# Kernel optimization log

Measured on AMD Instinct MI355X. Metric: run time of the kernel, lower is better.

Reference implementation:

```python
import jax, jax.numpy as jnp
import numpy as np

N = 100000   # nodes
E = 625000   # edges
D = 128      # feature dim (layers = [128,128,128])
H = 8        # attention heads
HD = 16      # head dim (H*HD == D)


def setup_inputs() -> dict:
    key = jax.random.key(0)
    ks = jax.random.split(key, 16)
    s = 1.0 / np.sqrt(D).astype(np.float32)
    inp = {
        'x': jax.random.normal(ks[0], (N, D), dtype=jnp.float32),
        'edge_index': jax.random.randint(ks[1], (2, E), 0, N, dtype=jnp.int64),
        'W1': jax.random.normal(ks[2], (D, D), dtype=jnp.float32) * s,
        'b1': jnp.zeros((D,), jnp.float32),
        'W2': jax.random.normal(ks[3], (D, D), dtype=jnp.float32) * s,
        'b2': jnp.zeros((D,), jnp.float32),
        'Wq': jax.random.normal(ks[4], (D, H * HD), dtype=jnp.float32) * s,
        'bq': jnp.zeros((H * HD,), jnp.float32),
        'Wk': jax.random.normal(ks[5], (D, H * HD), dtype=jnp.float32) * s,
        'bk': jnp.zeros((H * HD,), jnp.float32),
        'Wv': jax.random.normal(ks[6], (D, H * HD), dtype=jnp.float32) * s,
        'bv': jnp.zeros((H * HD,), jnp.float32),
        'Wo': jax.random.normal(ks[7], (H * HD, D), dtype=jnp.float32) * s,
        'bo': jnp.zeros((D,), jnp.float32),
    }
    return inp


def _gcn_conv(x, W, b, src, dst):
    """PyG GCNConv: x' = D^-1/2 (A+I) D^-1/2 (x W) + b, symmetric norm with self-loops."""
    h = x @ W                                   # [N, Dout]
    # degree at targets, +1 for self-loop
    deg = jnp.ones((N,), h.dtype).at[dst].add(jnp.ones((E,), h.dtype))
    dinv = jax.lax.rsqrt(deg)                   # [N]
    norm = dinv[src] * dinv[dst]                # [E]
    agg = jnp.zeros_like(h).at[dst].add(h[src] * norm[:, None])
    agg = agg + h * (dinv * dinv)[:, None]      # self-loop term
    return agg + b


def _mha_seq1(x, Wq, bq, Wk, bk, Wv, bv, Wo, bo):
    """Faithful to the hand-rolled MHA: batch=N, implied seq_len=1."""
    n = x.shape[0]
    q = (x @ Wq + bq).reshape(n, 1, H, HD).transpose(0, 2, 1, 3)  # [N,H,1,HD]
    k = (x @ Wk + bk).reshape(n, 1, H, HD).transpose(0, 2, 1, 3)
    v = (x @ Wv + bv).reshape(n, 1, H, HD).transpose(0, 2, 1, 3)
    scores = jnp.einsum('nhqd,nhkd->nhqk', q, k) / np.float32(np.sqrt(HD))
    attn = jax.nn.softmax(scores, axis=-1)                        # [N,H,1,1]
    out = jnp.einsum('nhqk,nhkd->nhqd', attn, v)                  # [N,H,1,HD]
    out = out.transpose(0, 2, 1, 3).reshape(n, 1, H * HD)
    return out @ Wo + bo                                          # [N,1,D]


def reference(x, edge_index, W1, b1, W2, b2, Wq, bq, Wk, bk, Wv, bv, Wo, bo):
    src, dst = edge_index[0], edge_index[1]
    h = _gcn_conv(x, W1, b1, src, dst)
    h = jax.nn.relu(h)                 # dropout is identity in eval
    h = _gcn_conv(h, W2, b2, src, dst) # last conv: no relu
    return _mha_seq1(h, Wq, bq, Wk, bk, Wv, bv, Wo, bo)
```

## Files before the change

### kernel.cpp

```cpp
#include <hip/hip_runtime.h>
#include <hip/hip_bf16.h>

#define DD 128
#define CAP 16
#define OVF_MAX 8192
#define ECHUNK 2048

typedef __bf16 bf16x8v __attribute__((ext_vector_type(8)));
typedef float  f32x4   __attribute__((ext_vector_type(4)));

__device__ inline unsigned short f2bf(float f) {
    unsigned u = __builtin_bit_cast(unsigned, f);
    unsigned r = (u + 0x7fffu + ((u >> 16) & 1u)) >> 16;
    return (unsigned short)r;
}
__device__ inline float bflo2f(unsigned p) { return __builtin_bit_cast(float, p << 16); }
__device__ inline float bfhi2f(unsigned p) { return __builtin_bit_cast(float, p & 0xffff0000u); }
__device__ inline float rl_f(int v, int i) {
    return __builtin_bit_cast(float, __builtin_amdgcn_readlane(v, i));
}

__global__ __launch_bounds__(256) void k_zero(int* __restrict__ a, int N) {
    int i = blockIdx.x * 256 + threadIdx.x;
    int stride = gridDim.x * 256;
    for (; i <= N; i += stride) a[i] = 0;
}

__global__ __launch_bounds__(256) void k_fill_fuse1(const int* __restrict__ src, const int* __restrict__ dst,
                                                    int* __restrict__ fillc, int* __restrict__ srcp,
                                                    int* __restrict__ ovfcnt, int2* __restrict__ ovf,
                                                    int E, int N, int FB,
                                                    const float* __restrict__ Wv, const float* __restrict__ Wo,
                                                    const float* __restrict__ bv, const float* __restrict__ bo,
                                                    float* __restrict__ Wf, float* __restrict__ bfo) {
    if ((int)blockIdx.x < FB) {
        int bin   = blockIdx.x & 7;
        int chunk = blockIdx.x >> 3;
        int binsz = (N + 7) / 8;
        int lo = bin * binsz;
        int hi = lo + binsz; if (hi > N) hi = N;
        int base = chunk * ECHUNK + threadIdx.x;
        #pragma unroll
        for (int i = 0; i < ECHUNK / 256; ++i) {
            int e = base + i * 256;
            if (e < E) {
                int d = dst[e];
                if (d >= lo && d < hi) {
                    int s = src[e];
                    if ((unsigned)s < (unsigned)N) {
                        int pos = atomicAdd(&fillc[d], 1);
                        if (pos < CAP) srcp[(size_t)d * CAP + pos] = s;
                        else {
                            int op = atomicAdd(ovfcnt, 1);
                            if (op < OVF_MAX) ovf[op] = make_int2(s, d);
                        }
                    }
                }
            }
        }
    } else {
        int gid = (blockIdx.x - FB) * 256 + threadIdx.x;
        if (gid >= (DD + 1) * DD) return;
        int i = gid >> 7, j = gid & (DD - 1);
        if (i < DD) {
            float acc = 0.f;
            for (int k = 0; k < DD; ++k) acc = fmaf(Wv[i * DD + k], Wo[k * DD + j], acc);
            Wf[i * DD + j] = acc;
        } else {
            float acc = bo[j];
            for (int k = 0; k < DD; ++k) acc = fmaf(bv[k], Wo[k * DD + j], acc);
            bfo[j] = acc;
        }
    }
}

__global__ __launch_bounds__(256) void k_dinv_wprep(const int* __restrict__ fillc, float* __restrict__ dinv,
                                                    int N, int nb,
                                                    const float* __restrict__ W2, const float* __restrict__ Wf,
                                                    const float* __restrict__ b2, const float* __restrict__ bfo,
                                                    unsigned short* __restrict__ W2ft, float* __restrict__ bf2,
                                                    const float* __restrict__ W1, unsigned short* __restrict__ Wt1) {
    if ((int)blockIdx.x < nb) {
        int n = blockIdx.x * 256 + threadIdx.x;
        if (n < N) dinv[n] = rsqrtf(1.0f + (float)fillc[n]);
    } else {
        int blk = blockIdx.x - nb;
        if (blk < 65) {
            int gid = blk * 256 + threadIdx.x;
            if (gid >= (DD + 1) * DD) return;
            int i = gid >> 7, j = gid & (DD - 1);
            if (i < DD) {
                float acc = 0.f;
                for (int k = 0; k < DD; ++k) acc = fmaf(W2[i * DD + k], Wf[k * DD + j], acc);
                W2ft[j * DD + i] = f2bf(acc);
            } else {
                float acc = bfo[j];
                for (int k = 0; k < DD; ++k) acc = fmaf(b2[k], Wf[k * DD + j], acc);
                bf2[j] = acc;
            }
        } else {
            int gid = (blk - 65) * 256 + threadIdx.x;
            int k = gid >> 7, n = gid & 127;
            Wt1[n * DD + k] = f2bf(W1[k * DD + n]);
        }
    }
}

template<int AF32>
__global__ __launch_bounds__(256, 2) void k_gemm_mfma(const void* __restrict__ Av,
                                                      const unsigned short* __restrict__ Wt,
                                                      unsigned short* __restrict__ Cb, int M) {
    int w  = threadIdx.x >> 6;
    int l  = threadIdx.x & 63;
    int lr = l & 15, lg = l >> 4;

    bf16x8v bfr[8][4];
    #pragma unroll
    for (int nt = 0; nt < 8; ++nt)
        #pragma unroll
        for (int kk = 0; kk < 4; ++kk)
            bfr[nt][kk] = *reinterpret_cast<const bf16x8v*>(Wt + (nt * 16 + lr) * DD + kk * 32 + lg * 8);

    int tiles = (M + 63) >> 6;
    for (int t = blockIdx.x; t < tiles; t += gridDim.x) {
        int m0 = t * 64 + w * 16;
        int row = m0 + lr;
        int rowc = row < M ? row : (M - 1);

        bf16x8v af[4];
        if (AF32) {
            const float* Af = (const float*)Av;
            #pragma unroll
            for (int kk = 0; kk < 4; ++kk) {
                const float* p = Af + (size_t)rowc * DD + kk * 32 + lg * 8;
                float4 u0 = *reinterpret_cast<const float4*>(p);
                float4 u1 = *reinterpret_cast<const float4*>(p + 4);
                af[kk][0] = (__bf16)u0.x; af[kk][1] = (__bf16)u0.y;
                af[kk][2] = (__bf16)u0.z; af[kk][3] = (__bf16)u0.w;
                af[kk][4] = (__bf16)u1.x; af[kk][5] = (__bf16)u1.y;
                af[kk][6] = (__bf16)u1.z; af[kk][7] = (__bf16)u1.w;
            }
        } else {
            const unsigned short* Ab = (const unsigned short*)Av;
            #pragma unroll
            for (int kk = 0; kk < 4; ++kk)
                af[kk] = *reinterpret_cast<const bf16x8v*>(Ab + (size_t)rowc * DD + kk * 32 + lg * 8);
        }

        f32x4 acc[8] = {};
        #pragma unroll
        for (int kk = 0; kk < 4; ++kk)
            #pragma unroll
            for (int nt = 0; nt < 8; ++nt)
                acc[nt] = __builtin_amdgcn_mfma_f32_16x16x32_bf16(af[kk], bfr[nt][kk], acc[nt], 0, 0, 0);

        #pragma unroll
        for (int nt = 0; nt < 8; ++nt)
            #pragma unroll
            for (int r = 0; r < 4; ++r) {
                int rr = m0 + lg * 4 + r;
                if (rr < M) Cb[(size_t)rr * DD + nt * 16 + lr] = f2bf(acc[nt][r]);
            }
    }
}

template<int OUTF32, int RELU>
__global__ __launch_bounds__(256) void k_gather_pad(const int* __restrict__ fillc, const int* __restrict__ srcp,
                                                    const float* __restrict__ dinv, const unsigned* __restrict__ h32,
                                                    const float* __restrict__ bias, void* __restrict__ outp,
                                                    int N, const int* __restrict__ ovfcnt, const int2* __restrict__ ovf) {
    int l = threadIdx.x & 63;
    int g = blockIdx.x * 4 + (threadIdx.x >> 6);
    int m0 = g * 4;
    if (m0 >= N) return;
    float2 bb = reinterpret_cast<const float2*>(bias)[l];

    int fcidx = m0 + l; if (fcidx >= N) fcidx = N - 1;
    int fc = (l < 4) ? fillc[fcidx] : 0;

    int deg[4], c[4], sv[4], wvb[4];
    #pragma unroll
    for (int r = 0; r < 4; ++r) {
        deg[r] = __builtin_amdgcn_readlane(fc, r);
        int cc = deg[r] > CAP ? CAP : deg[r];
        c[r] = cc;
        int row = (m0 + r < N) ? (m0 + r) : (N - 1);
        sv[r] = (cc > 0) ? srcp[(size_t)row * CAP + (l < cc ? l : cc - 1)] : 0;
    }
    #pragma unroll
    for (int r = 0; r < 4; ++r)
        wvb[r] = __builtin_bit_cast(int, dinv[sv[r]]);

    unsigned p[4][8]; float w[4][8];
    #pragma unroll
    for (int r = 0; r < 4; ++r) {
        int f = c[r] < 8 ? c[r] : 8;
        #pragma unroll
        for (int q = 0; q < 8; ++q) {
            int i = (q < f) ? q : (f > 0 ? f - 1 : 0);
            int s = __builtin_amdgcn_readlane(sv[r], i);
            p[r][q] = h32[(size_t)s * 64 + l];
            w[r][q] = (q < f) ? rl_f(wvb[r], i) : 0.f;
        }
    }
    unsigned ps[4];
    #pragma unroll
    for (int r = 0; r < 4; ++r) {
        int n = m0 + r; int nc = n < N ? n : N - 1;
        ps[r] = h32[(size_t)nc * 64 + l];
    }

    float ax[4] = {0.f, 0.f, 0.f, 0.f}, ay[4] = {0.f, 0.f, 0.f, 0.f};
    #pragma unroll
    for (int r = 0; r < 4; ++r)
        #pragma unroll
        for (int q = 0; q < 8; ++q) {
            ax[r] = fmaf(w[r][q], bflo2f(p[r][q]), ax[r]);
            ay[r] = fmaf(w[r][q], bfhi2f(p[r][q]), ay[r]);
        }

    #pragma unroll
    for (int r = 0; r < 4; ++r) {
        for (int i = 8; i < c[r]; i += 8) {
            #pragma unroll
            for (int q = 0; q < 8; ++q) {
                int ii = (i + q < c[r]) ? i + q : c[r] - 1;
                int s = __builtin_amdgcn_readlane(sv[r], ii);
                unsigned pp = h32[(size_t)s * 64 + l];
                float wq = (i + q < c[r]) ? rl_f(wvb[r], ii) : 0.f;
                ax[r] = fmaf(wq, bflo2f(pp), ax[r]);
                ay[r] = fmaf(wq, bfhi2f(pp), ay[r]);
            }
        }
    }

    int anyovf = 0;
    #pragma unroll
    for (int r = 0; r < 4; ++r) anyovf |= (deg[r] > CAP) ? 1 : 0;
    if (anyovf) {
        int oc = *ovfcnt; if (oc > OVF_MAX) oc = OVF_MAX;
        for (int i = 0; i < oc; ++i) {
            int2 e = ovf[i];
            #pragma unroll
            for (int r = 0; r < 4; ++r) {
                if (deg[r] > CAP && e.y == m0 + r) {
                    float wq = dinv[e.x];
                    unsigned pp = h32[(size_t)e.x * 64 + l];
                    ax[r] = fmaf(wq, bflo2f(pp), ax[r]);
                    ay[r] = fmaf(wq, bfhi2f(pp), ay[r]);
                }
            }
        }
    }

    #pragma unroll
    for (int r = 0; r < 4; ++r) {
        int n = m0 + r;
        if (n < N) {
            float di = rsqrtf(1.0f + (float)deg[r]);
            float di2 = di * di;
            float ox = fmaf(di2, bflo2f(ps[r]), di * ax[r]) + bb.x;
            float oy = fmaf(di2, bfhi2f(ps[r]), di * ay[r]) + bb.y;
            if (RELU) { ox = fmaxf(ox, 0.f); oy = fmaxf(oy, 0.f); }
            if (OUTF32) {
                reinterpret_cast<float2*>(outp)[(size_t)n * 64 + l] = make_float2(ox, oy);
            } else {
                unsigned po = (unsigned)f2bf(ox) | ((unsigned)f2bf(oy) << 16);
                reinterpret_cast<unsigned*>(outp)[(size_t)n * 64 + l] = po;
            }
        }
    }
}

extern "C" void kernel_launch(void* const* d_in, const int* in_sizes, int n_in,
                              void* d_out, int out_size, void* d_ws, size_t ws_size,
                              hipStream_t stream) {
    const float* x  = (const float*)d_in[0];
    const int*   ei = (const int*)d_in[1];
    const float* W1 = (const float*)d_in[2];
    const float* b1 = (const float*)d_in[3];
    const float* W2 = (const float*)d_in[4];
    const float* b2 = (const float*)d_in[5];
    const float* Wv = (const float*)d_in[10];
    const float* bv = (const float*)d_in[11];
    const float* Wo = (const float*)d_in[12];
    const float* bo = (const float*)d_in[13];
    int N = in_sizes[0] / DD;
    int E = in_sizes[1] / 2;
    const int* src = ei;
    const int* dst = ei + E;
    float* out = (float*)d_out;

    unsigned* hA  = (unsigned*)d_ws;
    unsigned* h1  = hA + (size_t)N * 64;
    float* dinv   = (float*)(h1 + (size_t)N * 64);
    float* Wf     = dinv + N;
    float* bfo    = Wf + DD * DD;
    float* bf2    = bfo + DD;
    unsigned short* Wt1  = (unsigned short*)(bf2 + DD);
    unsigned short* W2ft = Wt1 + DD * DD;
    int* fillc  = (int*)(W2ft + DD * DD);
    int* ovfcnt = fillc + N;
    int2* ovf   = (int2*)(((uintptr_t)(ovfcnt + 1) + 63) & ~(uintptr_t)63);
    int* srcp   = (int*)(((uintptr_t)(ovf + OVF_MAX) + 63) & ~(uintptr_t)63);

    int nb = (N + 255) / 256;
    int nchunks = (E + ECHUNK - 1) / ECHUNK;
    int FB = nchunks * 8;

    k_zero<<<512, 256, 0, stream>>>(fillc, N);
    k_fill_fuse1<<<FB + 129, 256, 0, stream>>>(src, dst, fillc, srcp, ovfcnt, ovf, E, N, FB,
                                               Wv, Wo, bv, bo, Wf, bfo);
    k_dinv_wprep<<<nb + 129, 256, 0, stream>>>(fillc, dinv, N, nb,
                                               W2, Wf, b2, bfo, W2ft, bf2, W1, Wt1);
    k_gemm_mfma<1><<<512, 256, 0, stream>>>(x, Wt1, (unsigned short*)hA, N);
    int nwaves = (N + 3) / 4;
    int gb = (nwaves + 3) / 4;
    k_gather_pad<0, 1><<<gb, 256, 0, stream>>>(fillc, srcp, dinv, hA, b1, h1, N, ovfcnt, ovf);
    k_gemm_mfma<0><<<512, 256, 0, stream>>>(h1, W2ft, (unsigned short*)hA, N);
    k_gather_pad<1, 0><<<gb, 256, 0, stream>>>(fillc, srcp, dinv, hA, bf2, out, N, ovfcnt, ovf);
}
```

Before: 165.8 us.

## Fuse first GCN gather with second-layer GEMM via LDS-staged MFMA

Merges the layer-1 aggregation kernel with the following W2 GEMM. Each 256-thread block aggregates 16 rows into shared memory as bf16, then runs MFMA against the full 128x128 weight matrix staged in LDS. This removes the h1 global round trip and one kernel launch. In exchange, every block reloads the 32KB weight tile from global/L2, and the larger LDS footprint (about 39KB per block) may lower occupancy for a latency-bound gather.

```diff
diff --git a/kernel.cpp b/kernel.cpp
--- a/kernel.cpp
+++ b/kernel.cpp
@@ -106,8 +106,7 @@
     }
 }
 
-template<int AF32>
-__global__ __launch_bounds__(256, 2) void k_gemm_mfma(const void* __restrict__ Av,
+__global__ __launch_bounds__(256, 2) void k_gemm_mfma(const float* __restrict__ Af,
                                                       const unsigned short* __restrict__ Wt,
                                                       unsigned short* __restrict__ Cb, int M) {
     int w  = threadIdx.x >> 6;
@@ -128,23 +127,15 @@
         int rowc = row < M ? row : (M - 1);
 
         bf16x8v af[4];
-        if (AF32) {
-            const float* Af = (const float*)Av;
-            #pragma unroll
-            for (int kk = 0; kk < 4; ++kk) {
-                const float* p = Af + (size_t)rowc * DD + kk * 32 + lg * 8;
-                float4 u0 = *reinterpret_cast<const float4*>(p);
-                float4 u1 = *reinterpret_cast<const float4*>(p + 4);
-                af[kk][0] = (__bf16)u0.x; af[kk][1] = (__bf16)u0.y;
-                af[kk][2] = (__bf16)u0.z; af[kk][3] = (__bf16)u0.w;
-                af[kk][4] = (__bf16)u1.x; af[kk][5] = (__bf16)u1.y;
-                af[kk][6] = (__bf16)u1.z; af[kk][7] = (__bf16)u1.w;
-            }
-        } else {
-            const unsigned short* Ab = (const unsigned short*)Av;
-            #pragma unroll
-            for (int kk = 0; kk < 4; ++kk)
-                af[kk] = *reinterpret_cast<const bf16x8v*>(Ab + (size_t)rowc * DD + kk * 32 + lg * 8);
+        #pragma unroll
+        for (int kk = 0; kk < 4; ++kk) {
+            const float* p = Af + (size_t)rowc * DD + kk * 32 + lg * 8;
+            float4 u0 = *reinterpret_cast<const float4*>(p);
+            float4 u1 = *reinterpret_cast<const float4*>(p + 4);
+            af[kk][0] = (__bf16)u0.x; af[kk][1] = (__bf16)u0.y;
+            af[kk][2] = (__bf16)u0.z; af[kk][3] = (__bf16)u0.w;
+            af[kk][4] = (__bf16)u1.x; af[kk][5] = (__bf16)u1.y;
+            af[kk][6] = (__bf16)u1.z; af[kk][7] = (__bf16)u1.w;
         }
 
         f32x4 acc[8] = {};
@@ -164,17 +155,28 @@
     }
 }
 
-template<int OUTF32, int RELU>
-__global__ __launch_bounds__(256) void k_gather_pad(const int* __restrict__ fillc, const int* __restrict__ srcp,
-                                                    const float* __restrict__ dinv, const unsigned* __restrict__ h32,
-                                                    const float* __restrict__ bias, void* __restrict__ outp,
-                                                    int N, const int* __restrict__ ovfcnt, const int2* __restrict__ ovf) {
-    int l = threadIdx.x & 63;
-    int g = blockIdx.x * 4 + (threadIdx.x >> 6);
-    int m0 = g * 4;
-    if (m0 >= N) return;
-    float2 bb = reinterpret_cast<const float2*>(bias)[l];
-
+__global__ __launch_bounds__(256) void k_gg(const int* __restrict__ fillc, const int* __restrict__ srcp,
+                                            const float* __restrict__ dinv, const unsigned* __restrict__ h32,
+                                            const float* __restrict__ b1, const unsigned short* __restrict__ W2ft,
+                                            unsigned short* __restrict__ hA2, int N,
+                                            const int* __restrict__ ovfcnt, const int2* __restrict__ ovf) {
+    __shared__ unsigned short Wl[128][136];
+    __shared__ unsigned short agg[16][136];
+    int t = threadIdx.x;
+    {
+        const unsigned* Wsrc = (const unsigned*)W2ft;
+        #pragma unroll
+        for (int i = 0; i < 32; ++i) {
+            int idx = t + i * 256;
+            int row = idx >> 6, col = idx & 63;
+            *reinterpret_cast<unsigned*>(&Wl[row][col * 2]) = Wsrc[idx];
+        }
+    }
+    int l = t & 63;
+    int w = t >> 6;
+    int m0 = blockIdx.x * 16 + w * 4;
+
+    float2 bb = reinterpret_cast<const float2*>(b1)[l];
     int fcidx = m0 + l; if (fcidx >= N) fcidx = N - 1;
     int fc = (l < 4) ? fillc[fcidx] : 0;
 
@@ -191,7 +193,7 @@
     for (int r = 0; r < 4; ++r)
         wvb[r] = __builtin_bit_cast(int, dinv[sv[r]]);
 
-    unsigned p[4][8]; float w[4][8];
+    unsigned p[4][8]; float wgt[4][8];
     #pragma unroll
     for (int r = 0; r < 4; ++r) {
         int f = c[r] < 8 ? c[r] : 8;
@@ -200,7 +202,7 @@
             int i = (q < f) ? q : (f > 0 ? f - 1 : 0);
             int s = __builtin_amdgcn_readlane(sv[r], i);
             p[r][q] = h32[(size_t)s * 64 + l];
-            w[r][q] = (q < f) ? rl_f(wvb[r], i) : 0.f;
+            wgt[r][q] = (q < f) ? rl_f(wvb[r], i) : 0.f;
         }
     }
     unsigned ps[4];
@@ -215,10 +217,9 @@
     for (int r = 0; r < 4; ++r)
         #pragma unroll
         for (int q = 0; q < 8; ++q) {
-            ax[r] = fmaf(w[r][q], bflo2f(p[r][q]), ax[r]);
-            ay[r] = fmaf(w[r][q], bfhi2f(p[r][q]), ay[r]);
-        }
-
+            ax[r] = fmaf(wgt[r][q], bflo2f(p[r][q]), ax[r]);
+            ay[r] = fmaf(wgt[r][q], bfhi2f(p[r][q]), ay[r]);
+        }
     #pragma unroll
     for (int r = 0; r < 4; ++r) {
         for (int i = 8; i < c[r]; i += 8) {
@@ -233,7 +234,6 @@
             }
         }
     }
-
     int anyovf = 0;
     #pragma unroll
     for (int r = 0; r < 4; ++r) anyovf |= (deg[r] > CAP) ? 1 : 0;
@@ -252,7 +252,128 @@
             }
         }
     }
-
+    #pragma unroll
+    for (int r = 0; r < 4; ++r) {
+        int n = m0 + r;
+        float di = rsqrtf(1.0f + (float)deg[r]);
+        float di2 = di * di;
+        float ox = fmaf(di2, bflo2f(ps[r]), di * ax[r]) + bb.x;
+        float oy = fmaf(di2, bfhi2f(ps[r]), di * ay[r]) + bb.y;
+        ox = fmaxf(ox, 0.f); oy = fmaxf(oy, 0.f);
+        unsigned po = (n < N) ? ((unsigned)f2bf(ox) | ((unsigned)f2bf(oy) << 16)) : 0u;
+        *reinterpret_cast<unsigned*>(&agg[w * 4 + r][l * 2]) = po;
+    }
+    __syncthreads();
+
+    int lr = l & 15, lg = l >> 4;
+    f32x4 acc[2] = {};
+    #pragma unroll
+    for (int kk = 0; kk < 4; ++kk) {
+        bf16x8v af = *reinterpret_cast<const bf16x8v*>(&agg[lr][kk * 32 + lg * 8]);
+        #pragma unroll
+        for (int j = 0; j < 2; ++j) {
+            int nt = w * 2 + j;
+            bf16x8v bfrag = *reinterpret_cast<const bf16x8v*>(&Wl[nt * 16 + lr][kk * 32 + lg * 8]);
+            acc[j] = __builtin_amdgcn_mfma_f32_16x16x32_bf16(af, bfrag, acc[j], 0, 0, 0);
+        }
+    }
+    int mb = blockIdx.x * 16;
+    #pragma unroll
+    for (int j = 0; j < 2; ++j) {
+        int nt = w * 2 + j;
+        #pragma unroll
+        for (int r4 = 0; r4 < 4; ++r4) {
+            int rr = mb + lg * 4 + r4;
+            if (rr < N) hA2[(size_t)rr * DD + nt * 16 + lr] = f2bf(acc[j][r4]);
+        }
+    }
+}
+
+__global__ __launch_bounds__(256) void k_gather_pad(const int* __restrict__ fillc, const int* __restrict__ srcp,
+                                                    const float* __restrict__ dinv, const unsigned* __restrict__ h32,
+                                                    const float* __restrict__ bias, float* __restrict__ outp,
+                                                    int N, const int* __restrict__ ovfcnt, const int2* __restrict__ ovf) {
+    int l = threadIdx.x & 63;
+    int g = blockIdx.x * 4 + (threadIdx.x >> 6);
+    int m0 = g * 4;
+    if (m0 >= N) return;
+    float2 bb = reinterpret_cast<const float2*>(bias)[l];
+
+    int fcidx = m0 + l; if (fcidx >= N) fcidx = N - 1;
+    int fc = (l < 4) ? fillc[fcidx] : 0;
+
+    int deg[4], c[4], sv[4], wvb[4];
+    #pragma unroll
+    for (int r = 0; r < 4; ++r) {
+        deg[r] = __builtin_amdgcn_readlane(fc, r);
+        int cc = deg[r] > CAP ? CAP : deg[r];
+        c[r] = cc;
+        int row = (m0 + r < N) ? (m0 + r) : (N - 1);
+        sv[r] = (cc > 0) ? srcp[(size_t)row * CAP + (l < cc ? l : cc - 1)] : 0;
+    }
+    #pragma unroll
+    for (int r = 0; r < 4; ++r)
+        wvb[r] = __builtin_bit_cast(int, dinv[sv[r]]);
+
+    unsigned p[4][8]; float w[4][8];
+    #pragma unroll
+    for (int r = 0; r < 4; ++r) {
+        int f = c[r] < 8 ? c[r] : 8;
+        #pragma unroll
+        for (int q = 0; q < 8; ++q) {
+            int i = (q < f) ? q : (f > 0 ? f - 1 : 0);
+            int s = __builtin_amdgcn_readlane(sv[r], i);
+            p[r][q] = h32[(size_t)s * 64 + l];
+            w[r][q] = (q < f) ? rl_f(wvb[r], i) : 0.f;
+        }
+    }
+    unsigned ps[4];
+    #pragma unroll
+    for (int r = 0; r < 4; ++r) {
+        int n = m0 + r; int nc = n < N ? n : N - 1;
+        ps[r] = h32[(size_t)nc * 64 + l];
+    }
+
+    float ax[4] = {0.f, 0.f, 0.f, 0.f}, ay[4] = {0.f, 0.f, 0.f, 0.f};
+    #pragma unroll
+    for (int r = 0; r < 4; ++r)
+        #pragma unroll
+        for (int q = 0; q < 8; ++q) {
+            ax[r] = fmaf(w[r][q], bflo2f(p[r][q]), ax[r]);
+            ay[r] = fmaf(w[r][q], bfhi2f(p[r][q]), ay[r]);
+        }
+    #pragma unroll
+    for (int r = 0; r < 4; ++r) {
+        for (int i = 8; i < c[r]; i += 8) {
+            #pragma unroll
+            for (int q = 0; q < 8; ++q) {
+                int ii = (i + q < c[r]) ? i + q : c[r] - 1;
+                int s = __builtin_amdgcn_readlane(sv[r], ii);
+                unsigned pp = h32[(size_t)s * 64 + l];
+                float wq = (i + q < c[r]) ? rl_f(wvb[r], ii) : 0.f;
+                ax[r] = fmaf(wq, bflo2f(pp), ax[r]);
+                ay[r] = fmaf(wq, bfhi2f(pp), ay[r]);
+            }
+        }
+    }
+    int anyovf = 0;
+    #pragma unroll
+    for (int r = 0; r < 4; ++r) anyovf |= (deg[r] > CAP) ? 1 : 0;
+    if (anyovf) {
+        int oc = *ovfcnt; if (oc > OVF_MAX) oc = OVF_MAX;
+        for (int i = 0; i < oc; ++i) {
+            int2 e = ovf[i];
+            #pragma unroll
+            for (int r = 0; r < 4; ++r) {
+                if (deg[r] > CAP && e.y == m0 + r) {
+                    float wq = dinv[e.x];
+                    unsigned pp = h32[(size_t)e.x * 64 + l];
+                    ax[r] = fmaf(wq, bflo2f(pp), ax[r]);
+                    ay[r] = fmaf(wq, bfhi2f(pp), ay[r]);
+                }
+            }
+        }
+    }
     #pragma unroll
     for (int r = 0; r < 4; ++r) {
         int n = m0 + r;
@@ -261,13 +382,7 @@
             float di2 = di * di;
             float ox = fmaf(di2, bflo2f(ps[r]), di * ax[r]) + bb.x;
             float oy = fmaf(di2, bfhi2f(ps[r]), di * ay[r]) + bb.y;
-            if (RELU) { ox = fmaxf(ox, 0.f); oy = fmaxf(oy, 0.f); }
-            if (OUTF32) {
-                reinterpret_cast<float2*>(outp)[(size_t)n * 64 + l] = make_float2(ox, oy);
-            } else {
-                unsigned po = (unsigned)f2bf(ox) | ((unsigned)f2bf(oy) << 16);
-                reinterpret_cast<unsigned*>(outp)[(size_t)n * 64 + l] = po;
-            }
+            reinterpret_cast<float2*>(outp)[(size_t)n * 64 + l] = make_float2(ox, oy);
         }
     }
 }
@@ -292,8 +407,8 @@
     float* out = (float*)d_out;
 
     unsigned* hA  = (unsigned*)d_ws;
-    unsigned* h1  = hA + (size_t)N * 64;
-    float* dinv   = (float*)(h1 + (size_t)N * 64);
+    unsigned* hA2 = hA + (size_t)N * 64;
+    float* dinv   = (float*)(hA2 + (size_t)N * 64);
     float* Wf     = dinv + N;
     float* bfo    = Wf + DD * DD;
     float* bf2    = bfo + DD;
@@ -313,10 +428,9 @@
                                                Wv, Wo, bv, bo, Wf, bfo);
     k_dinv_wprep<<<nb + 129, 256, 0, stream>>>(fillc, dinv, N, nb,
                                                W2, Wf, b2, bfo, W2ft, bf2, W1, Wt1);
-    k_gemm_mfma<1><<<512, 256, 0, stream>>>(x, Wt1, (unsigned short*)hA, N);
-    int nwaves = (N + 3) / 4;
-    int gb = (nwaves + 3) / 4;
-    k_gather_pad<0, 1><<<gb, 256, 0, stream>>>(fillc, srcp, dinv, hA, b1, h1, N, ovfcnt, ovf);
-    k_gemm_mfma<0><<<512, 256, 0, stream>>>(h1, W2ft, (unsigned short*)hA, N);
-    k_gather_pad<1, 0><<<gb, 256, 0, stream>>>(fillc, srcp, dinv, hA, bf2, out, N, ovfcnt, ovf);
-}
+    k_gemm_mfma<<<512, 256, 0, stream>>>(x, Wt1, (unsigned short*)hA, N);
+    int ggb = (N + 15) / 16;
+    k_gg<<<ggb, 256, 0, stream>>>(fillc, srcp, dinv, hA, b1, W2ft, (unsigned short*)hA2, N, ovfcnt, ovf);
+    int gb = ((N + 3) / 4 + 3) / 4;
+    k_gather_pad<<<gb, 256, 0, stream>>>(fillc, srcp, dinv, hA2, bf2, out, N, ovfcnt, ovf);
+}
```

New measurement: 161.8 us. -2.4%, faster.
